# Performance work log

Measured on AMD Instinct MI355X. Metric: run time of the kernel, lower is better.

## Reference

```python
import jax, jax.numpy as jnp
import numpy as np

N_NODES = 40000
N_EDGES = 640000
N_GRAPHS = 64
DIM_IN = 32
N_EDGE_TYPE = 16
DH = 128
DOUT = 256
T = 4


def setup_inputs() -> dict:
    key = jax.random.key(0)
    ks = jax.random.split(key, 16)
    inp = {
        "x": jax.random.normal(ks[0], (N_NODES, DIM_IN), dtype=jnp.float32),
        "edge_index": jax.random.randint(ks[1], (2, N_EDGES), 0, N_NODES, dtype=jnp.int64),
        "edge_attr": jax.random.normal(ks[2], (N_EDGES, N_EDGE_TYPE), dtype=jnp.float32),
        "graph_ids": jnp.sort(jax.random.randint(ks[3], (N_NODES,), 0, N_GRAPHS, dtype=jnp.int64)),
    }
    s = lambda fan_in: 1.0 / np.sqrt(fan_in)
    inp["Wn"] = jax.random.uniform(ks[4], (DIM_IN, DH), jnp.float32, -s(DIM_IN), s(DIM_IN))
    inp["bn"] = jnp.zeros((DH,), jnp.float32)
    inp["We"] = jax.random.uniform(ks[5], (N_EDGE_TYPE, DH), jnp.float32, -s(N_EDGE_TYPE), s(N_EDGE_TYPE))
    inp["be"] = jnp.zeros((DH,), jnp.float32)
    inp["W1"] = jax.random.uniform(ks[6], (DH, DH), jnp.float32, -s(DH), s(DH))
    inp["b1"] = jnp.zeros((DH,), jnp.float32)
    inp["W2"] = jax.random.uniform(ks[7], (DH, DH), jnp.float32, -s(DH), s(DH))
    inp["b2"] = jnp.zeros((DH,), jnp.float32)
    inp["Wl"] = jax.random.uniform(ks[8], (DH * T, DOUT), jnp.float32, -s(DH * T), s(DH * T))
    inp["bl"] = jnp.zeros((DOUT,), jnp.float32)
    return inp


def reference(x, edge_index, edge_attr, graph_ids, Wn, bn, We, be, W1, b1, W2, b2, Wl, bl):
    # node / edge input transforms
    h = x @ Wn + bn                      # [N, DH]
    e = edge_attr @ We + be              # [E, DH]
    src, dst = edge_index[0], edge_index[1]

    def mlp(z):
        return jax.nn.relu(z @ W1 + b1) @ W2 + b2

    all_h = []
    for _ in range(T):
        # GINE: message = relu(x_src + edge_attr), scatter-sum to dst
        msg = jax.nn.relu(h[src] + e)                                 # [E, DH]
        agg = jax.ops.segment_sum(msg, dst, num_segments=N_NODES)     # [N, DH]
        h = mlp(h + agg)                                              # eps = 0 -> (1+eps)*x = x
        all_h.append(h)

    all_x = jnp.concatenate(all_h, axis=-1)                           # [N, DH*T]
    pooled = jax.ops.segment_sum(all_x, graph_ids, num_segments=N_GRAPHS)  # [G, DH*T]
    return pooled @ Wl + bl                                           # [G, DOUT]
```

## Files before the change

### kernel.cpp

```cpp
#include <hip/hip_runtime.h>

#define N_NODES   40000
#define N_EDGES   640000
#define N_GRAPHS  64
#define DIM_IN    32
#define N_ETYPE   16
#define DH        128
#define DOUT      256
#define T_ITERS   4
#define SCAN_BLK  40

typedef unsigned int uint32;
typedef unsigned short ushort16;
typedef __attribute__((ext_vector_type(8))) short bf16x8;
typedef __attribute__((ext_vector_type(4))) float f32x4;

__device__ __forceinline__ uint32 f2bf1(float f) {
  uint32 u = __float_as_uint(f);
  return (u + 0x7fffu + ((u >> 16) & 1u)) >> 16;
}
__device__ __forceinline__ uint32 pack_bf2(float lo, float hi) {
  return (f2bf1(hi) << 16) | f2bf1(lo);
}

__global__ __launch_bounds__(256) void k_embed(const float* __restrict__ x,
                                               const float* __restrict__ Wn,
                                               const float* __restrict__ bn,
                                               float* __restrict__ h,
                                               ushort16* __restrict__ hb) {
  int idx = blockIdx.x * 256 + threadIdx.x;
  int n = idx >> 7, c = idx & 127;
  const float* xr = x + n * DIM_IN;
  float acc = bn[c];
#pragma unroll
  for (int k = 0; k < DIM_IN; ++k)
    acc = fmaf(xr[k], Wn[k * DH + c], acc);
  h[idx] = acc;
  hb[idx] = (ushort16)f2bf1(acc);
}

__global__ __launch_bounds__(256) void k_hist(const int* __restrict__ dst,
                                              int* __restrict__ counts) {
  int i = blockIdx.x * 256 + threadIdx.x;
  atomicAdd(&counts[dst[i]], 1);
}

__global__ __launch_bounds__(1024) void k_scan1(const int* __restrict__ counts,
                                                int* __restrict__ excl,
                                                int* __restrict__ blk_sums) {
  __shared__ int wsums[16];
  int tid = threadIdx.x, lane = tid & 63, w = tid >> 6;
  int i = blockIdx.x * 1024 + tid;
  int v = (i < N_NODES) ? counts[i] : 0;
  int s = v;
#pragma unroll
  for (int off = 1; off < 64; off <<= 1) {
    int t = __shfl_up(s, off);
    if (lane >= off) s += t;
  }
  if (lane == 63) wsums[w] = s;
  __syncthreads();
  if (tid < 16) {
    int ws_ = wsums[tid];
#pragma unroll
    for (int off = 1; off < 16; off <<= 1) {
      int t = __shfl_up(ws_, off);
      if (tid >= off) ws_ += t;
    }
    wsums[tid] = ws_;
  }
  __syncthreads();
  int e = s - v + (w ? wsums[w - 1] : 0);
  if (i < N_NODES) excl[i] = e;
  if (tid == 0) blk_sums[blockIdx.x] = wsums[15];
}

__global__ __launch_bounds__(64) void k_scan2(const int* __restrict__ blk_sums,
                                              int* __restrict__ blk_off,
                                              int* __restrict__ row_start) {
  int lane = threadIdx.x;
  int v = (lane < SCAN_BLK) ? blk_sums[lane] : 0;
  int s = v;
#pragma unroll
  for (int off = 1; off < 64; off <<= 1) {
    int t = __shfl_up(s, off);
    if (lane >= off) s += t;
  }
  if (lane < SCAN_BLK) blk_off[lane] = s - v;
  if (lane == 63) row_start[N_NODES] = s;
}

__global__ __launch_bounds__(1024) void k_scan3(int* __restrict__ row_start,
                                                const int* __restrict__ blk_off,
                                                int* __restrict__ cursor) {
  int i = blockIdx.x * 1024 + threadIdx.x;
  if (i < N_NODES) {
    int v = row_start[i] + blk_off[blockIdx.x];
    row_start[i] = v;
    cursor[i] = v;
  }
}

__global__ __launch_bounds__(256) void k_permute(const int* __restrict__ src,
                                                 const int* __restrict__ dst,
                                                 int* __restrict__ cursor,
                                                 int* __restrict__ src_perm,
                                                 int* __restrict__ eid_perm) {
  int i = blockIdx.x * 256 + threadIdx.x;
  int d = dst[i];
  int pos = atomicAdd(&cursor[d], 1);
  src_perm[pos] = src[i];
  eid_perm[pos] = i;
}

__global__ __launch_bounds__(256) void k_permute_ea(const int* __restrict__ src,
                                                    const int* __restrict__ dst,
                                                    const float4* __restrict__ edge_attr,
                                                    int* __restrict__ cursor,
                                                    int* __restrict__ src_perm,
                                                    float4* __restrict__ ea_perm) {
  int i = blockIdx.x * 256 + threadIdx.x;
  int d = dst[i];
  int pos = atomicAdd(&cursor[d], 1);
  src_perm[pos] = src[i];
  const float4* s = edge_attr + ((size_t)i << 2);
  float4* o = ea_perm + ((size_t)pos << 2);
  float4 v0 = s[0], v1 = s[1], v2 = s[2], v3 = s[3];
  o[0] = v0; o[1] = v1; o[2] = v2; o[3] = v3;
}

#define MAC16(A0,A1,A2,A3)                                          \
  p0 = fmaf(A0.x, we0[0], p0);  p1 = fmaf(A0.x, we1[0], p1);        \
  p0 = fmaf(A0.y, we0[1], p0);  p1 = fmaf(A0.y, we1[1], p1);        \
  p0 = fmaf(A0.z, we0[2], p0);  p1 = fmaf(A0.z, we1[2], p1);        \
  p0 = fmaf(A0.w, we0[3], p0);  p1 = fmaf(A0.w, we1[3], p1);        \
  p0 = fmaf(A1.x, we0[4], p0);  p1 = fmaf(A1.x, we1[4], p1);        \
  p0 = fmaf(A1.y, we0[5], p0);  p1 = fmaf(A1.y, we1[5], p1);        \
  p0 = fmaf(A1.z, we0[6], p0);  p1 = fmaf(A1.z, we1[6], p1);        \
  p0 = fmaf(A1.w, we0[7], p0);  p1 = fmaf(A1.w, we1[7], p1);        \
  p0 = fmaf(A2.x, we0[8], p0);  p1 = fmaf(A2.x, we1[8], p1);        \
  p0 = fmaf(A2.y, we0[9], p0);  p1 = fmaf(A2.y, we1[9], p1);        \
  p0 = fmaf(A2.z, we0[10], p0); p1 = fmaf(A2.z, we1[10], p1);       \
  p0 = fmaf(A2.w, we0[11], p0); p1 = fmaf(A2.w, we1[11], p1);       \
  p0 = fmaf(A3.x, we0[12], p0); p1 = fmaf(A3.x, we1[12], p1);       \
  p0 = fmaf(A3.y, we0[13], p0); p1 = fmaf(A3.y, we1[13], p1);       \
  p0 = fmaf(A3.z, we0[14], p0); p1 = fmaf(A3.z, we1[14], p1);       \
  p0 = fmaf(A3.w, we0[15], p0); p1 = fmaf(A3.w, we1[15], p1);

#define RELU_ACC(G)                                                  \
  acc0 += fmaxf(__uint_as_float((G) << 16) + p0, 0.0f);              \
  acc1 += fmaxf(__uint_as_float((G) & 0xffff0000u) + p1, 0.0f);

#define ACC2(G,E)                                                                 \
  acc0 += fmaxf(__uint_as_float((G) << 16) + __uint_as_float((E) << 16), 0.0f);   \
  acc1 += fmaxf(__uint_as_float((G) & 0xffff0000u) +                              \
                __uint_as_float((E) & 0xffff0000u), 0.0f);

__global__ __launch_bounds__(256) void k_perm_e(const int* __restrict__ src,
                                                const int* __restrict__ dst,
                                                const float4* __restrict__ edge_attr,
                                                const float* __restrict__ We,
                                                const float* __restrict__ be,
                                                int* __restrict__ cursor,
                                                int* __restrict__ src_perm,
                                                uint32* __restrict__ e_perm) {
  __shared__ float4 sAttr[1024];
  __shared__ int spos[256];
  int tid = threadIdx.x;
  int i = blockIdx.x * 256 + tid;
  int d = dst[i];
  int pos = atomicAdd(&cursor[d], 1);
  src_perm[pos] = src[i];
  spos[tid] = pos;
  size_t blockBase = (size_t)blockIdx.x * 1024;
  for (int idx = tid; idx < 1024; idx += 256)
    sAttr[idx] = edge_attr[blockBase + idx];
  __syncthreads();
  int lane = tid & 63, wv = tid >> 6;
  int c = lane << 1;
  float we0[N_ETYPE], we1[N_ETYPE];
#pragma unroll
  for (int k = 0; k < N_ETYPE; ++k) {
    we0[k] = We[k * DH + c];
    we1[k] = We[k * DH + c + 1];
  }
  float be0 = be[c], be1 = be[c + 1];
  const float4* a = &sAttr[wv << 8];
  const int* wp = &spos[wv << 6];
#pragma unroll 2
  for (int j = 0; j < 64; ++j) {
    int pos_j = wp[j];
    float4 a0 = a[j * 4 + 0], a1 = a[j * 4 + 1], a2 = a[j * 4 + 2], a3 = a[j * 4 + 3];
    float p0 = be0, p1 = be1;
    MAC16(a0, a1, a2, a3)
    e_perm[((size_t)pos_j << 6) + lane] = pack_bf2(p0, p1);
  }
}

__global__ __launch_bounds__(256) void k_prep_w(const float* __restrict__ W1,
                                                const float* __restrict__ W2,
                                                ushort16* __restrict__ w1c,
                                                ushort16* __restrict__ w2c) {
  int id = blockIdx.x * 256 + threadIdx.x;
  int which = id >> 14;
  int rem = id & 16383;
  int j = rem & 7, lg = (rem >> 3) & 63, n = (rem >> 9) & 7, k0 = rem >> 12;
  int r = lg & 15, g = lg >> 4;
  const float* W = which ? W2 : W1;
  ushort16* wc = which ? w2c : w1c;
  wc[rem] = (ushort16)f2bf1(W[(k0 * 32 + g * 8 + j) * 128 + n * 16 + r]);
}

__global__ __launch_bounds__(256) void k_fused(const uint32* __restrict__ hb_cur,
                                               const uint32* __restrict__ e_perm,
                                               const int* __restrict__ row_start,
                                               const int* __restrict__ src_perm,
                                               const ushort16* __restrict__ w1c,
                                               const ushort16* __restrict__ w2c,
                                               const float* __restrict__ b1,
                                               const float* __restrict__ b2,
                                               const int* __restrict__ graph_ids,
                                               uint32* __restrict__ hb_nxt,
                                               float* __restrict__ pooled,
                                               int t_slot) {
  __shared__ ushort16 sA[64 * 136];
  int tid = threadIdx.x;
  int rb = blockIdx.x * 64;
  int l = tid & 63, w = tid >> 6;

  for (int j = 0; j < 16; ++j) {
    int n = rb + w * 16 + j;
    uint32 hself = hb_cur[(size_t)n * 64 + l];
    float acc0 = __uint_as_float(hself << 16);
    float acc1 = __uint_as_float(hself & 0xffff0000u);
    int beg = row_start[n], end = row_start[n + 1];
    const uint32* ep = e_perm + ((size_t)beg << 6) + l;
    const int* sp = src_perm + beg;
    int m = end - beg;
    int i = 0;
    for (; i + 8 <= m; i += 8, ep += 512, sp += 8) {
      int ss[8]; uint32 gg[8], ee[8];
#pragma unroll
      for (int k = 0; k < 8; ++k) ss[k] = sp[k];
#pragma unroll
      for (int k = 0; k < 8; ++k) gg[k] = hb_cur[((size_t)ss[k] << 6) + l];
#pragma unroll
      for (int k = 0; k < 8; ++k) ee[k] = ep[k * 64];
#pragma unroll
      for (int k = 0; k < 8; ++k) { ACC2(gg[k], ee[k]) }
    }
    for (; i + 2 <= m; i += 2, ep += 128, sp += 2) {
      int s0 = sp[0], s1 = sp[1];
      uint32 g0 = hb_cur[((size_t)s0 << 6) + l];
      uint32 g1 = hb_cur[((size_t)s1 << 6) + l];
      uint32 e0 = ep[0], e1 = ep[64];
      ACC2(g0, e0) ACC2(g1, e1)
    }
    for (; i < m; ++i, ep += 64, ++sp) {
      int s0 = sp[0];
      uint32 g0 = hb_cur[((size_t)s0 << 6) + l];
      uint32 e0 = ep[0];
      ACC2(g0, e0)
    }
    *(uint32*)&sA[(w * 16 + j) * 136 + 2 * l] = pack_bf2(acc0, acc1);
  }

  int r = l & 15, g = l >> 4;
  const ushort16* aBase = &sA[0] + (w * 16 + r) * 136 + g * 8;

  f32x4 acc[8];
#pragma unroll
  for (int n = 0; n < 8; ++n) {
    float bv = b1[n * 16 + r];
    acc[n] = (f32x4){bv, bv, bv, bv};
  }
#pragma unroll
  for (int k0 = 0; k0 < 4; ++k0) {
    bf16x8 a = *(const bf16x8*)(aBase + k0 * 32);
#pragma unroll
    for (int n = 0; n < 8; ++n) {
      bf16x8 b = *(const bf16x8*)(w1c + (k0 * 8 + n) * 512 + l * 8);
      acc[n] = __builtin_amdgcn_mfma_f32_16x16x32_bf16(a, b, acc[n], 0, 0, 0);
    }
  }

#pragma unroll
  for (int n = 0; n < 8; ++n)
#pragma unroll
    for (int q = 0; q < 4; ++q)
      sA[(w * 16 + g * 4 + q) * 136 + n * 16 + r] = (ushort16)f2bf1(fmaxf(acc[n][q], 0.0f));

#pragma unroll
  for (int n = 0; n < 8; ++n) {
    float bv = b2[n * 16 + r];
    acc[n] = (f32x4){bv, bv, bv, bv};
  }
#pragma unroll
  for (int k0 = 0; k0 < 4; ++k0) {
    bf16x8 a = *(const bf16x8*)(aBase + k0 * 32);
#pragma unroll
    for (int n = 0; n < 8; ++n) {
      bf16x8 b = *(const bf16x8*)(w2c + (k0 * 8 + n) * 512 + l * 8);
      acc[n] = __builtin_amdgcn_mfma_f32_16x16x32_bf16(a, b, acc[n], 0, 0, 0);
    }
  }

  float* pbase = pooled + t_slot * DH;
  int node0 = rb + w * 16;
  int gid0 = graph_ids[node0];
  if (gid0 == graph_ids[node0 + 15]) {
#pragma unroll
    for (int n = 0; n < 8; ++n) {
      float s = acc[n][0] + acc[n][1] + acc[n][2] + acc[n][3];
      s += __shfl_xor(s, 16);
      s += __shfl_xor(s, 32);
      if (l < 16) atomicAdd(&pbase[gid0 * 512 + n * 16 + r], s);
    }
  } else {
#pragma unroll
    for (int q = 0; q < 4; ++q) {
      int node = node0 + g * 4 + q;
      int gg = graph_ids[node];
#pragma unroll
      for (int n = 0; n < 8; ++n)
        atomicAdd(&pbase[gg * 512 + n * 16 + r], acc[n][q]);
    }
  }

#pragma unroll
  for (int n = 0; n < 8; ++n)
#pragma unroll
    for (int q = 0; q < 4; ++q)
      sA[(w * 16 + g * 4 + q) * 136 + n * 16 + r] = (ushort16)f2bf1(acc[n][q]);
  __syncthreads();
  for (int idx = tid; idx < 4096; idx += 256) {
    int row = idx >> 6, dw = idx & 63;
    uint32 v = *(const uint32*)&sA[row * 136 + dw * 2];
    hb_nxt[(size_t)(rb + row) * 64 + dw] = v;
  }
}

__global__ __launch_bounds__(256) void k_agg_seq(const float* __restrict__ h,
                                                 const uint32* __restrict__ hb,
                                                 const float4* __restrict__ ea_perm,
                                                 const float* __restrict__ We,
                                                 const float* __restrict__ be,
                                                 const int* __restrict__ row_start,
                                                 const int* __restrict__ src_perm,
                                                 float* __restrict__ z) {
  int lane = threadIdx.x & 63;
  int n = (blockIdx.x << 2) + (threadIdx.x >> 6);
  int c = lane << 1;
  float we0[N_ETYPE], we1[N_ETYPE];
#pragma unroll
  for (int k = 0; k < N_ETYPE; ++k) {
    we0[k] = We[k * DH + c];
    we1[k] = We[k * DH + c + 1];
  }
  float be0 = be[c], be1 = be[c + 1];
  float2 hself = *(const float2*)&h[(size_t)n * DH + c];
  float acc0 = hself.x, acc1 = hself.y;
  int beg = row_start[n], end = row_start[n + 1];
  const float4* ea = ea_perm + ((size_t)beg << 2);
  int i = beg;
  for (; i + 4 <= end; i += 4, ea += 16) {
    int s0 = src_perm[i], s1 = src_perm[i + 1], s2 = src_perm[i + 2], s3 = src_perm[i + 3];
    uint32 g0 = hb[((size_t)s0 << 6) + lane];
    uint32 g1 = hb[((size_t)s1 << 6) + lane];
    uint32 g2 = hb[((size_t)s2 << 6) + lane];
    uint32 g3 = hb[((size_t)s3 << 6) + lane];
    float4 a0 = ea[0], a1 = ea[1], a2 = ea[2], a3 = ea[3];
    float4 b0 = ea[4], b1v = ea[5], b2v = ea[6], b3 = ea[7];
    float p0, p1;
    p0 = be0; p1 = be1; MAC16(a0, a1, a2, a3) RELU_ACC(g0)
    p0 = be0; p1 = be1; MAC16(b0, b1v, b2v, b3) RELU_ACC(g1)
    a0 = ea[8]; a1 = ea[9]; a2 = ea[10]; a3 = ea[11];
    b0 = ea[12]; b1v = ea[13]; b2v = ea[14]; b3 = ea[15];
    p0 = be0; p1 = be1; MAC16(a0, a1, a2, a3) RELU_ACC(g2)
    p0 = be0; p1 = be1; MAC16(b0, b1v, b2v, b3) RELU_ACC(g3)
  }
  for (; i < end; ++i, ea += 4) {
    int s0 = src_perm[i];
    uint32 g0 = hb[((size_t)s0 << 6) + lane];
    float4 a0 = ea[0], a1 = ea[1], a2 = ea[2], a3 = ea[3];
    float p0 = be0, p1 = be1;
    MAC16(a0, a1, a2, a3) RELU_ACC(g0)
  }
  *(float2*)&z[(size_t)n * DH + c] = make_float2(acc0, acc1);
}

__global__ __launch_bounds__(256, 8) void k_agg_ind(const float* __restrict__ h,
                                                    const uint32* __restrict__ hb,
                                                    const float* __restrict__ edge_attr,
                                                    const float* __restrict__ We,
                                                    const float* __restrict__ be,
                                                    const int* __restrict__ row_start,
                                                    const int* __restrict__ src_perm,
                                                    const int* __restrict__ eid_perm,
                                                    float* __restrict__ z) {
  int lane = threadIdx.x & 63;
  int n = (blockIdx.x << 2) + (threadIdx.x >> 6);
  int c = lane << 1;
  float we0[N_ETYPE], we1[N_ETYPE];
#pragma unroll
  for (int k = 0; k < N_ETYPE; ++k) {
    we0[k] = We[k * DH + c];
    we1[k] = We[k * DH + c + 1];
  }
  float be0 = be[c], be1 = be[c + 1];
  float2 hself = *(const float2*)&h[(size_t)n * DH + c];
  float acc0 = hself.x, acc1 = hself.y;
  int beg = row_start[n], end = row_start[n + 1];
  int i = beg;
  for (; i + 1 < end; i += 2) {
    int s0 = src_perm[i], s1 = src_perm[i + 1];
    int e0i = eid_perm[i], e1i = eid_perm[i + 1];
    uint32 g0 = hb[((size_t)s0 << 6) + lane];
    uint32 g1 = hb[((size_t)s1 << 6) + lane];
    const float4* eA = (const float4*)(edge_attr + (size_t)e0i * N_ETYPE);
    const float4* eB = (const float4*)(edge_attr + (size_t)e1i * N_ETYPE);
    float4 a0 = eA[0], a1 = eA[1], a2 = eA[2], a3 = eA[3];
    float p0, p1;
    p0 = be0; p1 = be1; MAC16(a0, a1, a2, a3) RELU_ACC(g0)
    float4 b0 = eB[0], b1v = eB[1], b2v = eB[2], b3 = eB[3];
    p0 = be0; p1 = be1; MAC16(b0, b1v, b2v, b3) RELU_ACC(g1)
  }
  if (i < end) {
    int s0 = src_perm[i];
    int e0i = eid_perm[i];
    uint32 g0 = hb[((size_t)s0 << 6) + lane];
    const float4* eA = (const float4*)(edge_attr + (size_t)e0i * N_ETYPE);
    float4 a0 = eA[0], a1 = eA[1], a2 = eA[2], a3 = eA[3];
    float p0 = be0, p1 = be1;
    MAC16(a0, a1, a2, a3) RELU_ACC(g0)
  }
  *(float2*)&z[(size_t)n * DH + c] = make_float2(acc0, acc1);
}

#define MLPFMA(K, U0, U1)                                            \
  {                                                                  \
    _Pragma("unroll")                                                \
    for (int i_ = 0; i_ < 8; ++i_) {                                 \
      float2 a_ = *(const float2*)&sA[(r0 + i_) * 132 + (K)];        \
      acc[i_][0] = fmaf(a_.x, U0.x, acc[i_][0]);                     \
      acc[i_][1] = fmaf(a_.x, U0.y, acc[i_][1]);                     \
      acc[i_][2] = fmaf(a_.x, U0.z, acc[i_][2]);                     \
      acc[i_][3] = fmaf(a_.x, U0.w, acc[i_][3]);                     \
      acc[i_][0] = fmaf(a_.y, U1.x, acc[i_][0]);                     \
      acc[i_][1] = fmaf(a_.y, U1.y, acc[i_][1]);                     \
      acc[i_][2] = fmaf(a_.y, U1.z, acc[i_][2]);                     \
      acc[i_][3] = fmaf(a_.y, U1.w, acc[i_][3]);                     \
    }                                                                \
  }

__device__ __forceinline__ void gemm_tile_g(const float* sA, const float4* __restrict__ Wv,
                                            float acc[8][4], int r0, int cg) {
  float4 c0 = Wv[cg],       c1 = Wv[32 + cg];
  float4 n0 = Wv[64 + cg],  n1 = Wv[96 + cg];
#pragma unroll 4
  for (int k = 0; k < DH - 4; k += 2) {
    float4 u0 = c0, u1 = c1;
    c0 = n0; c1 = n1;
    n0 = Wv[(k + 4) * 32 + cg];
    n1 = Wv[(k + 5) * 32 + cg];
    MLPFMA(k, u0, u1)
  }
  MLPFMA(DH - 4, c0, c1)
  MLPFMA(DH - 2, n0, n1)
}

__global__ __launch_bounds__(256) void k_mlp(const float* __restrict__ z,
                                             const float* __restrict__ W1,
                                             const float* __restrict__ b1,
                                             const float* __restrict__ W2,
                                             const float* __restrict__ b2,
                                             const int* __restrict__ graph_ids,
                                             float* __restrict__ h_out,
                                             uint32* __restrict__ hb_out,
                                             float* __restrict__ pooled,
                                             int t_slot) {
  __shared__ float sA[64 * 132];
  int tid = threadIdx.x;
  int rb = blockIdx.x * 64;
  for (int idx = tid; idx < 64 * 32; idx += 256) {
    int r = idx >> 5, kq = (idx & 31) << 2;
    *(float4*)&sA[r * 132 + kq] = *(const float4*)&z[(size_t)(rb + r) * DH + kq];
  }
  __syncthreads();

  int cg = tid & 31, rg = tid >> 5;
  int c0 = cg << 2, r0 = rg << 3;
  float acc[8][4];
  {
    float4 bb = *(const float4*)&b1[c0];
#pragma unroll
    for (int i = 0; i < 8; ++i) { acc[i][0] = bb.x; acc[i][1] = bb.y; acc[i][2] = bb.z; acc[i][3] = bb.w; }
  }
  gemm_tile_g(sA, (const float4*)W1, acc, r0, cg);
  __syncthreads();
#pragma unroll
  for (int i = 0; i < 8; ++i) {
    float4 v;
    v.x = fmaxf(acc[i][0], 0.0f); v.y = fmaxf(acc[i][1], 0.0f);
    v.z = fmaxf(acc[i][2], 0.0f); v.w = fmaxf(acc[i][3], 0.0f);
    *(float4*)&sA[(r0 + i) * 132 + c0] = v;
  }
  __syncthreads();
  {
    float4 bb = *(const float4*)&b2[c0];
#pragma unroll
    for (int i = 0; i < 8; ++i) { acc[i][0] = bb.x; acc[i][1] = bb.y; acc[i][2] = bb.z; acc[i][3] = bb.w; }
  }
  gemm_tile_g(sA, (const float4*)W2, acc, r0, cg);

  int node0 = rb + r0;
#pragma unroll
  for (int i = 0; i < 8; ++i) {
    float4 v = make_float4(acc[i][0], acc[i][1], acc[i][2], acc[i][3]);
    *(float4*)&h_out[(size_t)(node0 + i) * DH + c0] = v;
    uint2 hv;
    hv.x = pack_bf2(acc[i][0], acc[i][1]);
    hv.y = pack_bf2(acc[i][2], acc[i][3]);
    *(uint2*)&hb_out[(size_t)(node0 + i) * 64 + (c0 >> 1)] = hv;
  }
  float* pbase = pooled + t_slot * DH;
  int g_first = graph_ids[node0];
  int g_last = graph_ids[node0 + 7];
  if (g_first == g_last) {
    float s0 = 0.f, s1 = 0.f, s2 = 0.f, s3 = 0.f;
#pragma unroll
    for (int i = 0; i < 8; ++i) { s0 += acc[i][0]; s1 += acc[i][1]; s2 += acc[i][2]; s3 += acc[i][3]; }
    atomicAdd(&pbase[g_first * 512 + c0 + 0], s0);
    atomicAdd(&pbase[g_first * 512 + c0 + 1], s1);
    atomicAdd(&pbase[g_first * 512 + c0 + 2], s2);
    atomicAdd(&pbase[g_first * 512 + c0 + 3], s3);
  } else {
#pragma unroll
    for (int i = 0; i < 8; ++i) {
      int g = graph_ids[node0 + i];
      atomicAdd(&pbase[g * 512 + c0 + 0], acc[i][0]);
      atomicAdd(&pbase[g * 512 + c0 + 1], acc[i][1]);
      atomicAdd(&pbase[g * 512 + c0 + 2], acc[i][2]);
      atomicAdd(&pbase[g * 512 + c0 + 3], acc[i][3]);
    }
  }
}

__global__ __launch_bounds__(256) void k_final(const float* __restrict__ pooled,
                                               const float* __restrict__ Wl,
                                               const float* __restrict__ bl,
                                               float* __restrict__ out) {
  int g = blockIdx.x, o = threadIdx.x;
  __shared__ float sp[DH * T_ITERS];
  for (int idx = o; idx < DH * T_ITERS; idx += 256) sp[idx] = pooled[g * (DH * T_ITERS) + idx];
  __syncthreads();
  float acc = bl[o];
#pragma unroll 8
  for (int j = 0; j < DH * T_ITERS; ++j)
    acc = fmaf(sp[j], Wl[j * DOUT + o], acc);
  out[g * DOUT + o] = acc;
}

extern "C" void kernel_launch(void* const* d_in, const int* in_sizes, int n_in,
                              void* d_out, int out_size, void* d_ws, size_t ws_size,
                              hipStream_t stream) {
  const float* x         = (const float*)d_in[0];
  const int*   edge_index= (const int*)d_in[1];
  const float* edge_attr = (const float*)d_in[2];
  const int*   graph_ids = (const int*)d_in[3];
  const float* Wn = (const float*)d_in[4];
  const float* bn = (const float*)d_in[5];
  const float* We = (const float*)d_in[6];
  const float* be = (const float*)d_in[7];
  const float* W1 = (const float*)d_in[8];
  const float* b1 = (const float*)d_in[9];
  const float* W2 = (const float*)d_in[10];
  const float* b2 = (const float*)d_in[11];
  const float* Wl = (const float*)d_in[12];
  const float* bl = (const float*)d_in[13];
  float* out = (float*)d_out;

  char* p = (char*)d_ws;
  auto alloc = [&](size_t bytes) { char* r = p; p += (bytes + 255) & ~(size_t)255; return r; };
  float*  h        = (float*)alloc((size_t)N_NODES * DH * 4);
  float*  z        = (float*)alloc((size_t)N_NODES * DH * 4);
  uint32* hb       = (uint32*)alloc((size_t)N_NODES * DH * 2);
  float*  pooled   = (float*)alloc((size_t)N_GRAPHS * DH * T_ITERS * 4);
  int*    counts   = (int*)alloc((size_t)N_NODES * 4);
  int*    row_start= (int*)alloc((size_t)(N_NODES + 1) * 4);
  int*    cursor   = (int*)alloc((size_t)N_NODES * 4);
  int*    src_perm = (int*)alloc((size_t)N_EDGES * 4);
  int*    blk_sums = (int*)alloc(256);
  int*    blk_off  = (int*)alloc(256);

  const int* src = edge_index;
  const int* dst = edge_index + N_EDGES;

  size_t used = (size_t)(p - (char*)d_ws);
  size_t need_e  = used + (size_t)N_EDGES * DH * 2 + 4096;
  size_t need_ea = used + (size_t)N_EDGES * N_ETYPE * 4 + 4096;

  hipMemsetAsync(counts, 0, (size_t)N_NODES * 4, stream);
  hipMemsetAsync(pooled, 0, (size_t)N_GRAPHS * DH * T_ITERS * 4, stream);

  k_embed<<<N_NODES * DH / 256, 256, 0, stream>>>(x, Wn, bn, h, (ushort16*)hb);
  k_hist<<<N_EDGES / 256, 256, 0, stream>>>(dst, counts);
  k_scan1<<<SCAN_BLK, 1024, 0, stream>>>(counts, row_start, blk_sums);
  k_scan2<<<1, 64, 0, stream>>>(blk_sums, blk_off, row_start);
  k_scan3<<<SCAN_BLK, 1024, 0, stream>>>(row_start, blk_off, cursor);

  if (ws_size >= need_e) {
    uint32* e_perm = (uint32*)alloc((size_t)N_EDGES * DH * 2);
    ushort16* w1c = (ushort16*)counts;
    ushort16* w2c = w1c + 16384;
    k_prep_w<<<128, 256, 0, stream>>>(W1, W2, w1c, w2c);
    k_perm_e<<<N_EDGES / 256, 256, 0, stream>>>(src, dst, (const float4*)edge_attr,
                                                We, be, cursor, src_perm, e_perm);
    uint32* hb_a = hb;
    uint32* hb_b = (uint32*)z;
    for (int t = 0; t < T_ITERS; ++t) {
      k_fused<<<N_NODES / 64, 256, 0, stream>>>(hb_a, e_perm, row_start, src_perm,
                                                w1c, w2c, b1, b2, graph_ids,
                                                hb_b, pooled, t);
      uint32* tmp = hb_a; hb_a = hb_b; hb_b = tmp;
    }
  } else if (ws_size >= need_ea) {
    float4* ea_perm = (float4*)alloc((size_t)N_EDGES * N_ETYPE * 4);
    k_permute_ea<<<N_EDGES / 256, 256, 0, stream>>>(src, dst, (const float4*)edge_attr,
                                                    cursor, src_perm, ea_perm);
    for (int t = 0; t < T_ITERS; ++t) {
      k_agg_seq<<<N_NODES / 4, 256, 0, stream>>>(h, hb, ea_perm, We, be, row_start, src_perm, z);
      k_mlp<<<N_NODES / 64, 256, 0, stream>>>(z, W1, b1, W2, b2, graph_ids, h, (uint32*)hb, pooled, t);
    }
  } else {
    int* eid_perm = (int*)alloc((size_t)N_EDGES * 4);
    k_permute<<<N_EDGES / 256, 256, 0, stream>>>(src, dst, cursor, src_perm, eid_perm);
    for (int t = 0; t < T_ITERS; ++t) {
      k_agg_ind<<<N_NODES / 4, 256, 0, stream>>>(h, (uint32*)hb, edge_attr, We, be, row_start, src_perm, eid_perm, z);
      k_mlp<<<N_NODES / 64, 256, 0, stream>>>(z, W1, b1, W2, b2, graph_ids, h, (uint32*)hb, pooled, t);
    }
  }
  k_final<<<N_GRAPHS, 256, 0, stream>>>(pooled, Wl, bl, out);
}
```

Measured before the change: 466.0 us.

## Recompute edge embeddings in aggregation instead of materializing bf16 edge features

Drops the path that precomputed a bf16 [E,128] edge-embedding array and ran one fused aggregate+MLP kernel. Instead it permutes the raw 16-wide edge attributes and recomputes edge_attr@We inside a one-wavefront-per-node aggregation kernel that writes bf16 z. A separate small-block MFMA MLP kernel then consumes z. This cuts per-iteration edge traffic from 256 bytes to 64 bytes per edge, at the cost of extra FMAs per edge and an extra launch and z round-trip per iteration.

```diff
diff --git a/kernel.cpp b/kernel.cpp
--- a/kernel.cpp
+++ b/kernel.cpp
@@ -151,203 +151,13 @@
   acc0 += fmaxf(__uint_as_float((G) << 16) + p0, 0.0f);              \
   acc1 += fmaxf(__uint_as_float((G) & 0xffff0000u) + p1, 0.0f);
 
-#define ACC2(G,E)                                                                 \
-  acc0 += fmaxf(__uint_as_float((G) << 16) + __uint_as_float((E) << 16), 0.0f);   \
-  acc1 += fmaxf(__uint_as_float((G) & 0xffff0000u) +                              \
-                __uint_as_float((E) & 0xffff0000u), 0.0f);
-
-__global__ __launch_bounds__(256) void k_perm_e(const int* __restrict__ src,
-                                                const int* __restrict__ dst,
-                                                const float4* __restrict__ edge_attr,
+__global__ __launch_bounds__(256) void k_agg_rc(const uint32* __restrict__ hb,
+                                                const float4* __restrict__ ea_perm,
                                                 const float* __restrict__ We,
                                                 const float* __restrict__ be,
-                                                int* __restrict__ cursor,
-                                                int* __restrict__ src_perm,
-                                                uint32* __restrict__ e_perm) {
-  __shared__ float4 sAttr[1024];
-  __shared__ int spos[256];
-  int tid = threadIdx.x;
-  int i = blockIdx.x * 256 + tid;
-  int d = dst[i];
-  int pos = atomicAdd(&cursor[d], 1);
-  src_perm[pos] = src[i];
-  spos[tid] = pos;
-  size_t blockBase = (size_t)blockIdx.x * 1024;
-  for (int idx = tid; idx < 1024; idx += 256)
-    sAttr[idx] = edge_attr[blockBase + idx];
-  __syncthreads();
-  int lane = tid & 63, wv = tid >> 6;
-  int c = lane << 1;
-  float we0[N_ETYPE], we1[N_ETYPE];
-#pragma unroll
-  for (int k = 0; k < N_ETYPE; ++k) {
-    we0[k] = We[k * DH + c];
-    we1[k] = We[k * DH + c + 1];
-  }
-  float be0 = be[c], be1 = be[c + 1];
-  const float4* a = &sAttr[wv << 8];
-  const int* wp = &spos[wv << 6];
-#pragma unroll 2
-  for (int j = 0; j < 64; ++j) {
-    int pos_j = wp[j];
-    float4 a0 = a[j * 4 + 0], a1 = a[j * 4 + 1], a2 = a[j * 4 + 2], a3 = a[j * 4 + 3];
-    float p0 = be0, p1 = be1;
-    MAC16(a0, a1, a2, a3)
-    e_perm[((size_t)pos_j << 6) + lane] = pack_bf2(p0, p1);
-  }
-}
-
-__global__ __launch_bounds__(256) void k_prep_w(const float* __restrict__ W1,
-                                                const float* __restrict__ W2,
-                                                ushort16* __restrict__ w1c,
-                                                ushort16* __restrict__ w2c) {
-  int id = blockIdx.x * 256 + threadIdx.x;
-  int which = id >> 14;
-  int rem = id & 16383;
-  int j = rem & 7, lg = (rem >> 3) & 63, n = (rem >> 9) & 7, k0 = rem >> 12;
-  int r = lg & 15, g = lg >> 4;
-  const float* W = which ? W2 : W1;
-  ushort16* wc = which ? w2c : w1c;
-  wc[rem] = (ushort16)f2bf1(W[(k0 * 32 + g * 8 + j) * 128 + n * 16 + r]);
-}
-
-__global__ __launch_bounds__(256) void k_fused(const uint32* __restrict__ hb_cur,
-                                               const uint32* __restrict__ e_perm,
-                                               const int* __restrict__ row_start,
-                                               const int* __restrict__ src_perm,
-                                               const ushort16* __restrict__ w1c,
-                                               const ushort16* __restrict__ w2c,
-                                               const float* __restrict__ b1,
-                                               const float* __restrict__ b2,
-                                               const int* __restrict__ graph_ids,
-                                               uint32* __restrict__ hb_nxt,
-                                               float* __restrict__ pooled,
-                                               int t_slot) {
-  __shared__ ushort16 sA[64 * 136];
-  int tid = threadIdx.x;
-  int rb = blockIdx.x * 64;
-  int l = tid & 63, w = tid >> 6;
-
-  for (int j = 0; j < 16; ++j) {
-    int n = rb + w * 16 + j;
-    uint32 hself = hb_cur[(size_t)n * 64 + l];
-    float acc0 = __uint_as_float(hself << 16);
-    float acc1 = __uint_as_float(hself & 0xffff0000u);
-    int beg = row_start[n], end = row_start[n + 1];
-    const uint32* ep = e_perm + ((size_t)beg << 6) + l;
-    const int* sp = src_perm + beg;
-    int m = end - beg;
-    int i = 0;
-    for (; i + 8 <= m; i += 8, ep += 512, sp += 8) {
-      int ss[8]; uint32 gg[8], ee[8];
-#pragma unroll
-      for (int k = 0; k < 8; ++k) ss[k] = sp[k];
-#pragma unroll
-      for (int k = 0; k < 8; ++k) gg[k] = hb_cur[((size_t)ss[k] << 6) + l];
-#pragma unroll
-      for (int k = 0; k < 8; ++k) ee[k] = ep[k * 64];
-#pragma unroll
-      for (int k = 0; k < 8; ++k) { ACC2(gg[k], ee[k]) }
-    }
-    for (; i + 2 <= m; i += 2, ep += 128, sp += 2) {
-      int s0 = sp[0], s1 = sp[1];
-      uint32 g0 = hb_cur[((size_t)s0 << 6) + l];
-      uint32 g1 = hb_cur[((size_t)s1 << 6) + l];
-      uint32 e0 = ep[0], e1 = ep[64];
-      ACC2(g0, e0) ACC2(g1, e1)
-    }
-    for (; i < m; ++i, ep += 64, ++sp) {
-      int s0 = sp[0];
-      uint32 g0 = hb_cur[((size_t)s0 << 6) + l];
-      uint32 e0 = ep[0];
-      ACC2(g0, e0)
-    }
-    *(uint32*)&sA[(w * 16 + j) * 136 + 2 * l] = pack_bf2(acc0, acc1);
-  }
-
-  int r = l & 15, g = l >> 4;
-  const ushort16* aBase = &sA[0] + (w * 16 + r) * 136 + g * 8;
-
-  f32x4 acc[8];
-#pragma unroll
-  for (int n = 0; n < 8; ++n) {
-    float bv = b1[n * 16 + r];
-    acc[n] = (f32x4){bv, bv, bv, bv};
-  }
-#pragma unroll
-  for (int k0 = 0; k0 < 4; ++k0) {
-    bf16x8 a = *(const bf16x8*)(aBase + k0 * 32);
-#pragma unroll
-    for (int n = 0; n < 8; ++n) {
-      bf16x8 b = *(const bf16x8*)(w1c + (k0 * 8 + n) * 512 + l * 8);
-      acc[n] = __builtin_amdgcn_mfma_f32_16x16x32_bf16(a, b, acc[n], 0, 0, 0);
-    }
-  }
-
-#pragma unroll
-  for (int n = 0; n < 8; ++n)
-#pragma unroll
-    for (int q = 0; q < 4; ++q)
-      sA[(w * 16 + g * 4 + q) * 136 + n * 16 + r] = (ushort16)f2bf1(fmaxf(acc[n][q], 0.0f));
-
-#pragma unroll
-  for (int n = 0; n < 8; ++n) {
-    float bv = b2[n * 16 + r];
-    acc[n] = (f32x4){bv, bv, bv, bv};
-  }
-#pragma unroll
-  for (int k0 = 0; k0 < 4; ++k0) {
-    bf16x8 a = *(const bf16x8*)(aBase + k0 * 32);
-#pragma unroll
-    for (int n = 0; n < 8; ++n) {
-      bf16x8 b = *(const bf16x8*)(w2c + (k0 * 8 + n) * 512 + l * 8);
-      acc[n] = __builtin_amdgcn_mfma_f32_16x16x32_bf16(a, b, acc[n], 0, 0, 0);
-    }
-  }
-
-  float* pbase = pooled + t_slot * DH;
-  int node0 = rb + w * 16;
-  int gid0 = graph_ids[node0];
-  if (gid0 == graph_ids[node0 + 15]) {
-#pragma unroll
-    for (int n = 0; n < 8; ++n) {
-      float s = acc[n][0] + acc[n][1] + acc[n][2] + acc[n][3];
-      s += __shfl_xor(s, 16);
-      s += __shfl_xor(s, 32);
-      if (l < 16) atomicAdd(&pbase[gid0 * 512 + n * 16 + r], s);
-    }
-  } else {
-#pragma unroll
-    for (int q = 0; q < 4; ++q) {
-      int node = node0 + g * 4 + q;
-      int gg = graph_ids[node];
-#pragma unroll
-      for (int n = 0; n < 8; ++n)
-        atomicAdd(&pbase[gg * 512 + n * 16 + r], acc[n][q]);
-    }
-  }
-
-#pragma unroll
-  for (int n = 0; n < 8; ++n)
-#pragma unroll
-    for (int q = 0; q < 4; ++q)
-      sA[(w * 16 + g * 4 + q) * 136 + n * 16 + r] = (ushort16)f2bf1(acc[n][q]);
-  __syncthreads();
-  for (int idx = tid; idx < 4096; idx += 256) {
-    int row = idx >> 6, dw = idx & 63;
-    uint32 v = *(const uint32*)&sA[row * 136 + dw * 2];
-    hb_nxt[(size_t)(rb + row) * 64 + dw] = v;
-  }
-}
-
-__global__ __launch_bounds__(256) void k_agg_seq(const float* __restrict__ h,
-                                                 const uint32* __restrict__ hb,
-                                                 const float4* __restrict__ ea_perm,
-                                                 const float* __restrict__ We,
-                                                 const float* __restrict__ be,
-                                                 const int* __restrict__ row_start,
-                                                 const int* __restrict__ src_perm,
-                                                 float* __restrict__ z) {
+                                                const int* __restrict__ row_start,
+                                                const int* __restrict__ src_perm,
+                                                uint32* __restrict__ zb) {
   int lane = threadIdx.x & 63;
   int n = (blockIdx.x << 2) + (threadIdx.x >> 6);
   int c = lane << 1;
@@ -358,8 +168,9 @@
     we1[k] = We[k * DH + c + 1];
   }
   float be0 = be[c], be1 = be[c + 1];
-  float2 hself = *(const float2*)&h[(size_t)n * DH + c];
-  float acc0 = hself.x, acc1 = hself.y;
+  uint32 hself = hb[(size_t)n * 64 + lane];
+  float acc0 = __uint_as_float(hself << 16);
+  float acc1 = __uint_as_float(hself & 0xffff0000u);
   int beg = row_start[n], end = row_start[n + 1];
   const float4* ea = ea_perm + ((size_t)beg << 2);
   int i = beg;
@@ -386,7 +197,117 @@
     float p0 = be0, p1 = be1;
     MAC16(a0, a1, a2, a3) RELU_ACC(g0)
   }
-  *(float2*)&z[(size_t)n * DH + c] = make_float2(acc0, acc1);
+  zb[(size_t)n * 64 + lane] = pack_bf2(acc0, acc1);
+}
+
+__global__ __launch_bounds__(256) void k_prep_w(const float* __restrict__ W1,
+                                                const float* __restrict__ W2,
+                                                ushort16* __restrict__ w1c,
+                                                ushort16* __restrict__ w2c) {
+  int id = blockIdx.x * 256 + threadIdx.x;
+  int which = id >> 14;
+  int rem = id & 16383;
+  int j = rem & 7, lg = (rem >> 3) & 63, n = (rem >> 9) & 7, k0 = rem >> 12;
+  int r = lg & 15, g = lg >> 4;
+  const float* W = which ? W2 : W1;
+  ushort16* wc = which ? w2c : w1c;
+  wc[rem] = (ushort16)f2bf1(W[(k0 * 32 + g * 8 + j) * 128 + n * 16 + r]);
+}
+
+__global__ __launch_bounds__(64) void k_mlp2(const uint32* __restrict__ zb,
+                                             const ushort16* __restrict__ w1c,
+                                             const ushort16* __restrict__ w2c,
+                                             const float* __restrict__ b1,
+                                             const float* __restrict__ b2,
+                                             const int* __restrict__ graph_ids,
+                                             uint32* __restrict__ hb_out,
+                                             float* __restrict__ pooled,
+                                             int t_slot) {
+  __shared__ ushort16 sA[16 * 136];
+  int l = threadIdx.x;
+  int rb = blockIdx.x * 16;
+
+  for (int idx = l; idx < 256; idx += 64) {
+    int row = idx >> 4, ch = idx & 15;
+    *(uint4*)&sA[row * 136 + ch * 8] = *(const uint4*)&zb[(size_t)(rb + row) * 64 + ch * 4];
+  }
+  __syncthreads();
+
+  int r = l & 15, g = l >> 4;
+  const ushort16* aBase = &sA[0] + r * 136 + g * 8;
+
+  f32x4 acc[8];
+#pragma unroll
+  for (int n = 0; n < 8; ++n) {
+    float bv = b1[n * 16 + r];
+    acc[n] = (f32x4){bv, bv, bv, bv};
+  }
+#pragma unroll
+  for (int k0 = 0; k0 < 4; ++k0) {
+    bf16x8 a = *(const bf16x8*)(aBase + k0 * 32);
+#pragma unroll
+    for (int n = 0; n < 8; ++n) {
+      bf16x8 b = *(const bf16x8*)(w1c + (k0 * 8 + n) * 512 + l * 8);
+      acc[n] = __builtin_amdgcn_mfma_f32_16x16x32_bf16(a, b, acc[n], 0, 0, 0);
+    }
+  }
+
+  __syncthreads();
+#pragma unroll
+  for (int n = 0; n < 8; ++n)
+#pragma unroll
+    for (int q = 0; q < 4; ++q)
+      sA[(g * 4 + q) * 136 + n * 16 + r] = (ushort16)f2bf1(fmaxf(acc[n][q], 0.0f));
+  __syncthreads();
+
+#pragma unroll
+  for (int n = 0; n < 8; ++n) {
+    float bv = b2[n * 16 + r];
+    acc[n] = (f32x4){bv, bv, bv, bv};
+  }
+#pragma unroll
+  for (int k0 = 0; k0 < 4; ++k0) {
+    bf16x8 a = *(const bf16x8*)(aBase + k0 * 32);
+#pragma unroll
+    for (int n = 0; n < 8; ++n) {
+      bf16x8 b = *(const bf16x8*)(w2c + (k0 * 8 + n) * 512 + l * 8);
+      acc[n] = __builtin_amdgcn_mfma_f32_16x16x32_bf16(a, b, acc[n], 0, 0, 0);
+    }
+  }
+
+  float* pbase = pooled + t_slot * DH;
+  int gid0 = graph_ids[rb];
+  if (gid0 == graph_ids[rb + 15]) {
+#pragma unroll
+    for (int n = 0; n < 8; ++n) {
+      float s = acc[n][0] + acc[n][1] + acc[n][2] + acc[n][3];
+      s += __shfl_xor(s, 16);
+      s += __shfl_xor(s, 32);
+      if (l < 16) atomicAdd(&pbase[gid0 * 512 + n * 16 + r], s);
+    }
+  } else {
+#pragma unroll
+    for (int q = 0; q < 4; ++q) {
+      int node = rb + g * 4 + q;
+      int gg = graph_ids[node];
+#pragma unroll
+      for (int n = 0; n < 8; ++n)
+        atomicAdd(&pbase[gg * 512 + n * 16 + r], acc[n][q]);
+    }
+  }
+
+  __syncthreads();
+#pragma unroll
+  for (int n = 0; n < 8; ++n)
+#pragma unroll
+    for (int q = 0; q < 4; ++q)
+      sA[(g * 4 + q) * 136 + n * 16 + r] = (ushort16)f2bf1(acc[n][q]);
+  __syncthreads();
+  for (int idx = l; idx < 1024; idx += 64) {
+    int row = idx >> 6, dw = idx & 63;
+    uint32 v = *(const uint32*)&sA[row * 136 + dw * 2];
+    hb_out[(size_t)(rb + row) * 64 + dw] = v;
+  }
 }
 
 __global__ __launch_bounds__(256, 8) void k_agg_ind(const float* __restrict__ h,
@@ -597,7 +518,6 @@
   const int* dst = edge_index + N_EDGES;
 
   size_t used = (size_t)(p - (char*)d_ws);
-  size_t need_e  = used + (size_t)N_EDGES * DH * 2 + 4096;
   size_t need_ea = used + (size_t)N_EDGES * N_ETYPE * 4 + 4096;
 
   hipMemsetAsync(counts, 0, (size_t)N_NODES * 4, stream);
@@ -609,35 +529,25 @@
   k_scan2<<<1, 64, 0, stream>>>(blk_sums, blk_off, row_start);
   k_scan3<<<SCAN_BLK, 1024, 0, stream>>>(row_start, blk_off, cursor);
 
-  if (ws_size >= need_e) {
-    uint32* e_perm = (uint32*)alloc((size_t)N_EDGES * DH * 2);
+  if (ws_size >= need_ea) {
+    float4* ea_perm = (float4*)alloc((size_t)N_EDGES * N_ETYPE * 4);
+    uint32* zb = (uint32*)z;
     ushort16* w1c = (ushort16*)counts;
     ushort16* w2c = w1c + 16384;
     k_prep_w<<<128, 256, 0, stream>>>(W1, W2, w1c, w2c);
-    k_perm_e<<<N_EDGES / 256, 256, 0, stream>>>(src, dst, (const float4*)edge_attr,
-                                                We, be, cursor, src_perm, e_perm);
-    uint32* hb_a = hb;
-    uint32* hb_b = (uint32*)z;
-    for (int t = 0; t < T_ITERS; ++t) {
-      k_fused<<<N_NODES / 64, 256, 0, stream>>>(hb_a, e_perm, row_start, src_perm,
-                                                w1c, w2c, b1, b2, graph_ids,
-                                                hb_b, pooled, t);
-      uint32* tmp = hb_a; hb_a = hb_b; hb_b = tmp;
-    }
-  } else if (ws_size >= need_ea) {
-    float4* ea_perm = (float4*)alloc((size_t)N_EDGES * N_ETYPE * 4);
     k_permute_ea<<<N_EDGES / 256, 256, 0, stream>>>(src, dst, (const float4*)edge_attr,
                                                     cursor, src_perm, ea_perm);
     for (int t = 0; t < T_ITERS; ++t) {
-      k_agg_seq<<<N_NODES / 4, 256, 0, stream>>>(h, hb, ea_perm, We, be, row_start, src_perm, z);
-      k_mlp<<<N_NODES / 64, 256, 0, stream>>>(z, W1, b1, W2, b2, graph_ids, h, (uint32*)hb, pooled, t);
+      k_agg_rc<<<N_NODES / 4, 256, 0, stream>>>(hb, ea_perm, We, be, row_start, src_perm, zb);
+      k_mlp2<<<N_NODES / 16, 64, 0, stream>>>(zb, w1c, w2c, b1, b2, graph_ids,
+                                              hb, pooled, t);
     }
   } else {
     int* eid_perm = (int*)alloc((size_t)N_EDGES * 4);
     k_permute<<<N_EDGES / 256, 256, 0, stream>>>(src, dst, cursor, src_perm, eid_perm);
     for (int t = 0; t < T_ITERS; ++t) {
-      k_agg_ind<<<N_NODES / 4, 256, 0, stream>>>(h, (uint32*)hb, edge_attr, We, be, row_start, src_perm, eid_perm, z);
-      k_mlp<<<N_NODES / 64, 256, 0, stream>>>(z, W1, b1, W2, b2, graph_ids, h, (uint32*)hb, pooled, t);
+      k_agg_ind<<<N_NODES / 4, 256, 0, stream>>>(h, hb, edge_attr, We, be, row_start, src_perm, eid_perm, z);
+      k_mlp<<<N_NODES / 64, 256, 0, stream>>>(z, W1, b1, W2, b2, graph_ids, h, hb, pooled, t);
     }
   }
   k_final<<<N_GRAPHS, 256, 0, stream>>>(pooled, Wl, bl, out);
```

After: 743.7 us. 1.6x slower.
